# Kernel tuning notes

Hardware: AMD Instinct MI355X
Metric: run time of the kernel (lower is better)

The kernel has to match this reference:

```python
import jax, jax.numpy as jnp
import numpy as np

EPS = 1e-5
KEEP_FRAC = 0.925


def conv1x1(x, w, b):
    # x: [B,C,H,W], w: [O,C], b: [O]
    return jnp.einsum('bchw,oc->bohw', x, w) + b[None, :, None, None]


def adain_norm(x):
    m = x.mean(axis=(2, 3), keepdims=True)
    v = x.var(axis=(2, 3), keepdims=True)
    return (x - m) / jnp.sqrt(v + EPS)


def zca_norm(x):
    B, C, H, W = x.shape
    f = x.reshape(B, C, H * W)
    m = f.mean(axis=-1, keepdims=True)
    fc = f - m
    cov = jnp.einsum('bcn,bdn->bcd', fc, fc) / (H * W - 1) + EPS * jnp.eye(C, dtype=x.dtype)
    s, U = jnp.linalg.eigh(cov)
    Ud = U * (1.0 / jnp.sqrt(s + EPS))[:, None, :]          # U @ diag(s^-1/2)
    whiten = jnp.einsum('bce,bde->bcd', Ud, U)              # U diag U^T
    out = jnp.einsum('bcd,bdn->bcn', whiten, fc)
    return out.reshape(B, C, H, W)


def correlation_block(xq, yk, wf, bf, wg, bg):
    B, C, H, W = xq.shape
    f = conv1x1(xq, wf, bf).reshape(B, C, -1)   # [B,C,n_x]
    g = conv1x1(yk, wg, bg).reshape(B, C, -1)   # [B,C,n_y]
    energy = jnp.einsum('bcn,bcm->bnm', f, g)   # f^T g : [B,n_x,n_y]
    corr = jax.nn.softmax(energy, axis=-1)
    atten = corr.mean(axis=1, keepdims=True)    # mean over n_x -> [B,1,n_y]
    return corr, atten


def attn_mask(a):
    # a: [B,1,n]; zero the positions of the k smallest values (union over batch, as in torch)
    n = a.shape[2]
    k = int(n * KEEP_FRAC)
    idx = jnp.argsort(a, axis=2)[:, :, :k]                   # smallest k per (b, channel)
    mask = jnp.ones_like(a).at[:, :, idx.reshape(-1)].set(0.0)
    return mask


def corr_mask(mx, my):
    # mx: [B,1,n_x], my: [B,1,n_y] -> equality mask [B,n_x,n_y]
    return (mx[:, 0, :, None] == my[:, 0, None, :]).astype(mx.dtype)


def savanet_forward(x, y, f_w, f_b, g_w, g_b, sa_f_w, sa_f_b, sa_g_w, sa_g_b, h_w, h_b, out_w, out_b):
    B, C, H, W = x.shape
    n = H * W
    x_adain = adain_norm(x)
    y_adain = adain_norm(y)
    x_zca = zca_norm(x)
    y_zca = zca_norm(y)
    correlation, _ = correlation_block(x_adain, y_adain, f_w, f_b, g_w, g_b)
    _, atten_x = correlation_block(x_zca, x_zca, sa_f_w, sa_f_b, sa_g_w, sa_g_b)
    _, atten_y = correlation_block(y_zca, y_zca, sa_f_w, sa_f_b, sa_g_w, sa_g_b)
    mx = attn_mask(atten_x)
    my = attn_mask(atten_y)
    cmask = corr_mask(mx, my)                               # [B,n,n]
    correlation = cmask * correlation
    l1 = jnp.clip(jnp.abs(correlation).sum(axis=2, keepdims=True), 1e-12, None)
    correlation = correlation / l1                          # F.normalize(p=1, dim=2)
    h = conv1x1(y, h_w, h_b).reshape(B, C, n)               # [B,C,n_y]
    residual = jnp.einsum('bcm,bnm->bcn', h, correlation)   # h @ corr^T -> [B,C,n_x]
    residual = residual.reshape(B, C, H, W)
    residual = conv1x1(residual, out_w, out_b)
    output = x + residual
    return output, atten_x, atten_y


def setup_inputs() -> dict:
    key = jax.random.key(0)
    ks = jax.random.split(key, 10)
    B, C, H, W = 2, 512, 64, 64
    scale = 0.02
    d = {
        'x': jax.random.normal(ks[0], (B, C, H, W), dtype=jnp.float32),
        'y': jax.random.normal(ks[1], (B, C, H, W), dtype=jnp.float32),
        'f_w': jax.random.normal(ks[2], (C, C), dtype=jnp.float32) * scale,
        'f_b': jnp.zeros((C,), dtype=jnp.float32),
        'g_w': jax.random.normal(ks[3], (C, C), dtype=jnp.float32) * scale,
        'g_b': jnp.zeros((C,), dtype=jnp.float32),
        'sa_f_w': jax.random.normal(ks[4], (C, C), dtype=jnp.float32) * scale,
        'sa_f_b': jnp.zeros((C,), dtype=jnp.float32),
        'sa_g_w': jax.random.normal(ks[5], (C, C), dtype=jnp.float32) * scale,
        'sa_g_b': jnp.zeros((C,), dtype=jnp.float32),
        'h_w': jax.random.normal(ks[6], (C, C), dtype=jnp.float32) * scale,
        'h_b': jnp.zeros((C,), dtype=jnp.float32),
        'out_w': jax.random.normal(ks[7], (C, C), dtype=jnp.float32) * scale,
        'out_b': jnp.zeros((C,), dtype=jnp.float32),
    }
    return d


def reference(x, y, f_w, f_b, g_w, g_b, sa_f_w, sa_f_b, sa_g_w, sa_g_b, h_w, h_b, out_w, out_b):
    return savanet_forward(x, y, f_w, f_b, g_w, g_b, sa_f_w, sa_f_b, sa_g_w, sa_g_b, h_w, h_b, out_w, out_b)
```

## Files before the change

kernel.cpp:

```cpp
#include <hip/hip_runtime.h>
#include <cstdint>

static constexpr int B2 = 2;
static constexpr int C = 512;
static constexpr int N = 4096;
static constexpr long CN = (long)C * N;
static constexpr long NC = (long)N * C;
static constexpr long CC = (long)C * C;
static constexpr long NN = (long)N * N;
static constexpr float EPSC = 1e-5f;
static constexpr int KSEL = 308;
static constexpr int NS_ITERS = 4;

typedef __attribute__((ext_vector_type(8))) __bf16 bf16x8;
typedef __attribute__((ext_vector_type(4))) float f32x4;

__device__ __forceinline__ float wredSum(float v){
#pragma unroll
  for (int o = 32; o >= 1; o >>= 1) v += __shfl_xor(v, o, 64);
  return v;
}

__device__ __forceinline__ void gld16(const __bf16* g, __bf16* l){
  __builtin_amdgcn_global_load_lds(
      (const __attribute__((address_space(1))) void*)g,
      (__attribute__((address_space(3))) void*)l, 16, 0, 0);
}

__device__ __forceinline__ void splitw(float v, __bf16* ph, __bf16* pl, long o){
  __bf16 h = (__bf16)v;
  ph[o] = h;
  pl[o] = (__bf16)(v - (float)h);
}

template<int PASSES, int TMH, int OUTMODE, int ROWP>
__global__ __launch_bounds__(256) void k_mm(
    const __bf16* __restrict__ Ah, const __bf16* __restrict__ Al,
    const __bf16* __restrict__ Bh, const __bf16* __restrict__ Bl,
    float* __restrict__ Cf, __bf16* __restrict__ Coh, __bf16* __restrict__ Col,
    int Nn, int K, long sAz, long sBz, long sCz,
    float alpha, const float* __restrict__ alpha_ptr,
    const float* __restrict__ brow, long sBr,
    const float* __restrict__ bcol, long sBc,
    const float* __restrict__ c0p,
    const float* __restrict__ addsrc, long sAddz,
    float* __restrict__ Pm, float* __restrict__ Ps)
{
  constexpr int NB = (PASSES == 3) ? 4 : 2;
  constexpr int SB = (PASSES == 3) ? 2 : 1;
  __shared__ __align__(16) __bf16 sm[NB][128 * 32];
  __shared__ float pmx[2][128], psx[2][128];
  const int z = blockIdx.z;
  const int nwx = gridDim.x;
  int lin = blockIdx.y * nwx + blockIdx.x;
  const int nwg = nwx * gridDim.y;
  if ((nwg & 7) == 0){
    const int cpx = nwg >> 3;
    lin = (lin & 7) * cpx + (lin >> 3);
  }
  const int i0 = (lin % nwx) * 128;
  const int j0 = (lin / nwx) * 128;
  const int tid = threadIdx.x;
  const int lane = tid & 63;
  const int w = tid >> 6;
  const int wr = (w >> 1) * 64, wc = (w & 1) * 64;
  const int lr = lane & 15;
  const int g = lane >> 4;

  const __bf16* pAh = Ah + (long)z * sAz + (long)i0 * K;
  const __bf16* pBh = Bh + (long)z * sBz + (long)j0 * K;
  const __bf16* pAl = (PASSES == 3) ? (Al + (long)z * sAz + (long)i0 * K) : nullptr;
  const __bf16* pBl = (PASSES == 3) ? (Bl + (long)z * sBz + (long)j0 * K) : nullptr;

  f32x4 acc[4][4] = {};

  for (int kt = 0; kt < K; kt += 32){
#pragma unroll
    for (int p = 0; p < 2; ++p){
      const int t2 = p * 256 + tid;
      const int row = t2 >> 2;
      const int gs = (t2 & 3) ^ ((row >> 1) & 3);
      const long go = (long)row * K + kt + gs * 8;
      gld16(pAh + go, &sm[0][t2 * 8]);
      gld16(pBh + go, &sm[SB][t2 * 8]);
      if constexpr (PASSES == 3){
        gld16(pAl + go, &sm[1][t2 * 8]);
        gld16(pBl + go, &sm[3][t2 * 8]);
      }
    }
    __syncthreads();
    bf16x8 fa[4], fal[4], fb[4], fbl[4];
#pragma unroll
    for (int mi = 0; mi < 4; ++mi){
      const int row = wr + mi * 16 + lr;
      const int off = row * 32 + ((g ^ ((row >> 1) & 3)) * 8);
      fa[mi] = *(const bf16x8*)(&sm[0][off]);
      if constexpr (PASSES == 3) fal[mi] = *(const bf16x8*)(&sm[1][off]);
    }
#pragma unroll
    for (int ni = 0; ni < 4; ++ni){
      const int row = wc + ni * 16 + lr;
      const int off = row * 32 + ((g ^ ((row >> 1) & 3)) * 8);
      fb[ni] = *(const bf16x8*)(&sm[SB][off]);
      if constexpr (PASSES == 3) fbl[ni] = *(const bf16x8*)(&sm[3][off]);
    }
#pragma unroll
    for (int mi = 0; mi < 4; ++mi)
#pragma unroll
      for (int ni = 0; ni < 4; ++ni){
        acc[mi][ni] = __builtin_amdgcn_mfma_f32_16x16x32_bf16(fa[mi], fb[ni], acc[mi][ni], 0, 0, 0);
        if constexpr (PASSES == 3){
          acc[mi][ni] = __builtin_amdgcn_mfma_f32_16x16x32_bf16(fa[mi],  fbl[ni], acc[mi][ni], 0, 0, 0);
          acc[mi][ni] = __builtin_amdgcn_mfma_f32_16x16x32_bf16(fal[mi], fb[ni],  acc[mi][ni], 0, 0, 0);
        }
      }
    __syncthreads();
  }

  float al2 = alpha;
  if (alpha_ptr) al2 *= alpha_ptr[z];
  const float c0v = c0p ? c0p[z] : 0.f;
#pragma unroll
  for (int mi = 0; mi < 4; ++mi){
    float mrow[4] = {-3.4e38f, -3.4e38f, -3.4e38f, -3.4e38f};
    float srow[4] = {0.f, 0.f, 0.f, 0.f};
#pragma unroll
    for (int ni = 0; ni < 4; ++ni){
      const int col = j0 + wc + ni * 16 + lr;
      const float bc = (bcol ? bcol[z * sBc + col] : 0.f) + c0v;
#pragma unroll
      for (int j = 0; j < 4; ++j){
        const int row = i0 + wr + mi * 16 + g * 4 + j;
        float v = acc[mi][ni][j] * al2;
        if (TMH) v = (((row == col) ? 3.f : 0.f) - v) * 0.5f;
        if (brow) v += brow[z * sBr + row];
        v += bc;
        if (addsrc) v += addsrc[(long)z * sAddz + (long)row * Nn + col];
        const long o = (long)z * sCz + (long)row * Nn + col;
        if (OUTMODE == 0){ Cf[o] = v; }
        else if (OUTMODE == 1){ __bf16 h = (__bf16)v; Coh[o] = h; Col[o] = (__bf16)(v - (float)h); }
        else { Coh[o] = (__bf16)v; }
        if constexpr (ROWP){
          if (v > mrow[j]){ srow[j] *= __expf(mrow[j] - v); mrow[j] = v; }
          srow[j] += __expf(v - mrow[j]);
        }
      }
    }
    if constexpr (ROWP){
#pragma unroll
      for (int j = 0; j < 4; ++j){
        float m = mrow[j], s = srow[j];
#pragma unroll
        for (int o = 1; o <= 8; o <<= 1){
          const float mo = __shfl_xor(m, o, 64);
          const float so = __shfl_xor(s, o, 64);
          const float nm = fmaxf(m, mo);
          s = s * __expf(m - nm) + so * __expf(mo - nm);
          m = nm;
        }
        if (lr == 0){
          const int rl = wr + mi * 16 + g * 4 + j;
          pmx[w & 1][rl] = m;
          psx[w & 1][rl] = s;
        }
      }
    }
  }
  if constexpr (ROWP){
    __syncthreads();
    if (tid < 128){
      const float m0 = pmx[0][tid], s0 = psx[0][tid];
      const float m1 = pmx[1][tid], s1 = psx[1][tid];
      const float nm = fmaxf(m0, m1);
      const float s = s0 * __expf(m0 - nm) + s1 * __expf(m1 - nm);
      Pm[(long)(j0 >> 7) * N + i0 + tid] = nm;
      Ps[(long)(j0 >> 7) * N + i0 + tid] = s;
    }
  }
}

template<int TMH, int OUTMODE, int NSYZ>
__global__ __launch_bounds__(256) void k_mm64(
    const __bf16* __restrict__ Ah, const __bf16* __restrict__ Al,
    const __bf16* __restrict__ Bh, const __bf16* __restrict__ Bl,
    const __bf16* __restrict__ tH, const __bf16* __restrict__ tL,
    float* __restrict__ Cf, __bf16* __restrict__ Coh, __bf16* __restrict__ Col,
    int Nn, int K, long sAz, long sBz, long sCz, float alpha)
{
  __shared__ __align__(16) __bf16 sm[4][64 * 64];
  const int z = blockIdx.z;
  const __bf16 *bAh, *bAl, *bBh, *bBl;
  long oC;
  if constexpr (NSYZ){
    if (z < 4){
      bAh = Ah + (long)z * CC; bAl = Al + (long)z * CC;
      bBh = tH + (long)z * CC; bBl = tL + (long)z * CC;
      oC = (long)z * CC;
    } else {
      const int zz = z - 4;
      bAh = tH + (long)zz * CC; bAl = tL + (long)zz * CC;
      bBh = Ah + (long)(4 + zz) * CC; bBl = Al + (long)(4 + zz) * CC;
      oC = (long)(4 + zz) * CC;
    }
  } else {
    bAh = Ah + (long)z * sAz; bAl = Al + (long)z * sAz;
    bBh = Bh + (long)z * sBz; bBl = Bl + (long)z * sBz;
    oC = (long)z * sCz;
  }
  const int i0 = blockIdx.x * 64;
  const int j0 = blockIdx.y * 64;
  const int tid = threadIdx.x;
  const int lane = tid & 63;
  const int w = tid >> 6;
  const int wr = (w >> 1) * 32, wc = (w & 1) * 32;
  const int lr = lane & 15;
  const int g = lane >> 4;

  const __bf16* pAh = bAh + (long)i0 * K;
  const __bf16* pAl = bAl + (long)i0 * K;
  const __bf16* pBh = bBh + (long)j0 * K;
  const __bf16* pBl = bBl + (long)j0 * K;

  f32x4 acc[2][2] = {};

  for (int kt = 0; kt < K; kt += 64){
#pragma unroll
    for (int p = 0; p < 2; ++p){
      const int t2 = p * 256 + tid;
      const int row = t2 >> 3;
      const int gs = (t2 & 7) ^ (row & 7);
      const long go = (long)row * K + kt + gs * 8;
      gld16(pAh + go, &sm[0][t2 * 8]);
      gld16(pAl + go, &sm[1][t2 * 8]);
      gld16(pBh + go, &sm[2][t2 * 8]);
      gld16(pBl + go, &sm[3][t2 * 8]);
    }
    __syncthreads();
#pragma unroll
    for (int ks = 0; ks < 2; ++ks){
      bf16x8 fa[2], fal[2], fb[2], fbl[2];
#pragma unroll
      for (int mi = 0; mi < 2; ++mi){
        const int row = wr + mi * 16 + lr;
        const int off = row * 64 + (((ks * 4 + g) ^ (row & 7)) * 8);
        fa[mi]  = *(const bf16x8*)(&sm[0][off]);
        fal[mi] = *(const bf16x8*)(&sm[1][off]);
      }
#pragma unroll
      for (int ni = 0; ni < 2; ++ni){
        const int row = wc + ni * 16 + lr;
        const int off = row * 64 + (((ks * 4 + g) ^ (row & 7)) * 8);
        fb[ni]  = *(const bf16x8*)(&sm[2][off]);
        fbl[ni] = *(const bf16x8*)(&sm[3][off]);
      }
#pragma unroll
      for (int mi = 0; mi < 2; ++mi)
#pragma unroll
        for (int ni = 0; ni < 2; ++ni){
          acc[mi][ni] = __builtin_amdgcn_mfma_f32_16x16x32_bf16(fa[mi],  fb[ni],  acc[mi][ni], 0, 0, 0);
          acc[mi][ni] = __builtin_amdgcn_mfma_f32_16x16x32_bf16(fa[mi],  fbl[ni], acc[mi][ni], 0, 0, 0);
          acc[mi][ni] = __builtin_amdgcn_mfma_f32_16x16x32_bf16(fal[mi], fb[ni],  acc[mi][ni], 0, 0, 0);
        }
    }
    __syncthreads();
  }

#pragma unroll
  for (int mi = 0; mi < 2; ++mi){
#pragma unroll
    for (int ni = 0; ni < 2; ++ni){
      const int col = j0 + wc + ni * 16 + lr;
#pragma unroll
      for (int j = 0; j < 4; ++j){
        const int row = i0 + wr + mi * 16 + g * 4 + j;
        float v = acc[mi][ni][j] * alpha;
        if (TMH) v = (((row == col) ? 3.f : 0.f) - v) * 0.5f;
        const long o = oC + (long)row * Nn + col;
        if (OUTMODE == 0){ Cf[o] = v; }
        else { __bf16 h = (__bf16)v; Coh[o] = h; Col[o] = (__bf16)(v - (float)h); }
      }
    }
  }
}

__global__ __launch_bounds__(256) void k_pv(
    const __bf16* __restrict__ E, const __bf16* __restrict__ Bh,
    const float* __restrict__ rm, const float* __restrict__ rsc,
    const float* __restrict__ mxv, const float* __restrict__ myv,
    __bf16* __restrict__ resH)
{
  __shared__ __align__(16) __bf16 sa[64 * 64];
  __shared__ __align__(16) __bf16 sb[128 * 64];
  const int z = blockIdx.z;
  int lin = blockIdx.y * 64 + blockIdx.x;
  lin = (lin & 7) * 32 + (lin >> 3);
  const int n0 = (lin & 63) * 64;
  const int c0 = (lin >> 6) * 128;
  const int tid = threadIdx.x;
  const int lane = tid & 63;
  const int w = tid >> 6;
  const int wr = (w >> 1) * 32, wc = (w & 1) * 64;
  const int lr = lane & 15, g = lane >> 4;

  const __bf16* pe = E + (long)z * NN + (long)n0 * N;
  const __bf16* pB = Bh + (long)z * CN + (long)c0 * N;

  const int ar = tid >> 2;
  const int slot = tid & 3;
  const float rmv = rm[(long)z * N + n0 + ar];
  const float rsv = rsc[(long)z * N + n0 + ar];
  const float tgt = mxv[n0 + ar];
  const __bf16* per = pe + (long)ar * N;

  f32x4 acc[2][4] = {};

  for (int kt = 0; kt < N; kt += 64){
#pragma unroll
    for (int d = 0; d < 2; ++d){
      const int gd = slot * 2 + d;
      const bf16x8 ev = *(const bf16x8*)(per + kt + gd * 8);
      const float4 m0 = *(const float4*)(myv + kt + gd * 8);
      const float4 m1 = *(const float4*)(myv + kt + gd * 8 + 4);
      bf16x8 pk;
      pk[0] = (__bf16)((m0.x == tgt) ? __expf((float)ev[0] - rmv) * rsv : 0.f);
      pk[1] = (__bf16)((m0.y == tgt) ? __expf((float)ev[1] - rmv) * rsv : 0.f);
      pk[2] = (__bf16)((m0.z == tgt) ? __expf((float)ev[2] - rmv) * rsv : 0.f);
      pk[3] = (__bf16)((m0.w == tgt) ? __expf((float)ev[3] - rmv) * rsv : 0.f);
      pk[4] = (__bf16)((m1.x == tgt) ? __expf((float)ev[4] - rmv) * rsv : 0.f);
      pk[5] = (__bf16)((m1.y == tgt) ? __expf((float)ev[5] - rmv) * rsv : 0.f);
      pk[6] = (__bf16)((m1.z == tgt) ? __expf((float)ev[6] - rmv) * rsv : 0.f);
      pk[7] = (__bf16)((m1.w == tgt) ? __expf((float)ev[7] - rmv) * rsv : 0.f);
      *(bf16x8*)(&sa[ar * 64 + ((gd ^ (ar & 7)) * 8)]) = pk;
    }
#pragma unroll
    for (int p = 0; p < 4; ++p){
      const int t2 = p * 256 + tid;
      const int row = t2 >> 3;
      const int gs = (t2 & 7) ^ (row & 7);
      gld16(pB + (long)row * N + kt + gs * 8, &sb[t2 * 8]);
    }
    __syncthreads();
#pragma unroll
    for (int ks = 0; ks < 2; ++ks){
      bf16x8 fa[2], fb[4];
#pragma unroll
      for (int mi = 0; mi < 2; ++mi){
        const int row = wr + mi * 16 + lr;
        fa[mi] = *(const bf16x8*)(&sa[row * 64 + (((ks * 4 + g) ^ (row & 7)) * 8)]);
      }
#pragma unroll
      for (int ni = 0; ni < 4; ++ni){
        const int row = wc + ni * 16 + lr;
        fb[ni] = *(const bf16x8*)(&sb[row * 64 + (((ks * 4 + g) ^ (row & 7)) * 8)]);
      }
#pragma unroll
      for (int mi = 0; mi < 2; ++mi)
#pragma unroll
        for (int ni = 0; ni < 4; ++ni)
          acc[mi][ni] = __builtin_amdgcn_mfma_f32_16x16x32_bf16(fa[mi], fb[ni], acc[mi][ni], 0, 0, 0);
    }
    __syncthreads();
  }
#pragma unroll
  for (int mi = 0; mi < 2; ++mi)
#pragma unroll
    for (int ni = 0; ni < 4; ++ni){
      const int c = c0 + wc + ni * 16 + lr;
#pragma unroll
      for (int j = 0; j < 4; ++j){
        const int n = n0 + wr + mi * 16 + g * 4 + j;
        resH[(long)z * NC + (long)n * C + c] = (__bf16)acc[mi][ni][j];
      }
    }
}

__global__ __launch_bounds__(256) void k_wtw(const float* __restrict__ A, const float* __restrict__ B,
                                             float* __restrict__ C2, float alpha){
  __shared__ float sa[16][32], sb[16][32];
  const int i0 = blockIdx.x * 32, j0 = blockIdx.y * 32;
  const int t = threadIdx.x;
  const int ti = t & 15, tj = t >> 4;
  const int li = t & 31, lc = t >> 5;
  float acc[2][2] = {};
  for (int cb = 0; cb < C; cb += 16){
    sa[lc][li]     = A[(long)(cb + lc) * C + i0 + li];
    sa[lc + 8][li] = A[(long)(cb + lc + 8) * C + i0 + li];
    sb[lc][li]     = B[(long)(cb + lc) * C + j0 + li];
    sb[lc + 8][li] = B[(long)(cb + lc + 8) * C + j0 + li];
    __syncthreads();
#pragma unroll
    for (int c = 0; c < 16; ++c){
      const float a0 = sa[c][ti * 2], a1 = sa[c][ti * 2 + 1];
      const float b0 = sb[c][tj * 2], b1 = sb[c][tj * 2 + 1];
      acc[0][0] = fmaf(a0, b0, acc[0][0]); acc[0][1] = fmaf(a0, b1, acc[0][1]);
      acc[1][0] = fmaf(a1, b0, acc[1][0]); acc[1][1] = fmaf(a1, b1, acc[1][1]);
    }
    __syncthreads();
  }
#pragma unroll
  for (int r = 0; r < 2; ++r)
#pragma unroll
    for (int s = 0; s < 2; ++s)
      C2[(long)(i0 + ti * 2 + r) * C + j0 + tj * 2 + s] = acc[r][s] * alpha;
}

__global__ __launch_bounds__(256) void k_wtv(const float* __restrict__ W, const float* __restrict__ b,
                                             float* __restrict__ u){
  __shared__ float sb2[C];
  const int t = threadIdx.x;
  sb2[t] = b[t]; sb2[t + 256] = b[t + 256];
  __syncthreads();
  const int e = blockIdx.x * 256 + t;
  float acc = 0.f;
  for (int c = 0; c < C; ++c) acc = fmaf(W[(long)c * C + e], sb2[c], acc);
  u[e] = acc;
}

__global__ void k_dot2(const float* __restrict__ a1, const float* __restrict__ b1,
                       const float* __restrict__ a2, const float* __restrict__ b2,
                       float* __restrict__ c0m2, float* __restrict__ c0s4){
  const int t = threadIdx.x;
  float s1 = 0.f, s2 = 0.f;
  for (int i = t; i < C; i += 256){ s1 += a1[i] * b1[i]; s2 += a2[i] * b2[i]; }
  __shared__ float sh1[4], sh2[4];
  s1 = wredSum(s1); s2 = wredSum(s2);
  if ((t & 63) == 0){ sh1[t >> 6] = s1; sh2[t >> 6] = s2; }
  __syncthreads();
  if (t == 0){
    float d1 = sh1[0] + sh1[1] + sh1[2] + sh1[3];
    float d2 = sh2[0] + sh2[1] + sh2[2] + sh2[3];
    c0m2[0] = d1; c0m2[1] = d1;
    c0s4[0] = d2; c0s4[1] = d2; c0s4[2] = d2; c0s4[3] = d2;
  }
}

__global__ __launch_bounds__(256) void k_pixvec(const __bf16* __restrict__ X, const float* __restrict__ u,
                                                float* __restrict__ out){
  const int z = blockIdx.y;
  const int wv = threadIdx.x >> 6, lane = threadIdx.x & 63;
  const int n = blockIdx.x * 4 + wv;
  float acc = 0.f;
  for (int d = lane; d < C; d += 64) acc += (float)X[(long)z * NC + (long)n * C + d] * u[d];
  acc = wredSum(acc);
  if (lane == 0) out[(long)z * N + n] = acc;
}

__global__ __launch_bounds__(256) void k_stats(const float* __restrict__ x, const float* __restrict__ y,
                                               float* __restrict__ meanv, float* __restrict__ invs){
  const int bid = blockIdx.x;
  const int t = bid >> 9, c = bid & 511;
  const float* src = (t < 2 ? x : y) + (long)(t & 1) * CN + (long)c * N;
  const int tid = threadIdx.x;
  float s1 = 0.f, s2 = 0.f;
  for (int i = tid; i < N; i += 256){ float v = src[i]; s1 += v; s2 += v * v; }
  __shared__ float sh1[4], sh2[4];
  s1 = wredSum(s1); s2 = wredSum(s2);
  if ((tid & 63) == 0){ sh1[tid >> 6] = s1; sh2[tid >> 6] = s2; }
  __syncthreads();
  if (tid == 0){
    float m = (sh1[0] + sh1[1] + sh1[2] + sh1[3]) * (1.f / (float)N);
    float ex2 = (sh2[0] + sh2[1] + sh2[2] + sh2[3]) * (1.f / (float)N);
    float var = ex2 - m * m;
    meanv[t * C + c] = m;
    invs[t * C + c] = rsqrtf((var > 0.f ? var : 0.f) + EPSC);
  }
}

__global__ __launch_bounds__(256) void k_prep(const float* __restrict__ src,
                                              const float* __restrict__ meanv, const float* __restrict__ invs, int toff,
                                              __bf16* __restrict__ adH,
                                              __bf16* __restrict__ fcH, __bf16* __restrict__ fcL,
                                              __bf16* __restrict__ ccH, __bf16* __restrict__ ccL,
                                              __bf16* __restrict__ rwH){
  __shared__ float tile[64][65];
  const int z = blockIdx.z;
  const int n0 = blockIdx.x * 64;
  const int c0 = blockIdx.y * 64;
  const int tid = threadIdx.x;
  const int tx = tid & 63, ty = tid >> 6;
  const int tgt = toff + z;
#pragma unroll
  for (int it = 0; it < 16; ++it){
    const int cc = it * 4 + ty;
    const float v = src[(long)z * CN + (long)(c0 + cc) * N + n0 + tx];
    tile[cc][tx] = v;
    const float cen = v - meanv[tgt * C + c0 + cc];
    splitw(cen, ccH, ccL, (long)tgt * CN + (long)(c0 + cc) * N + n0 + tx);
  }
  __syncthreads();
  const float m = meanv[tgt * C + c0 + tx];
  const float r = invs[tgt * C + c0 + tx];
#pragma unroll
  for (int it = 0; it < 16; ++it){
    const int p = it * 4 + ty;
    const float v = tile[tx][p];
    const float cen = v - m;
    const long o = (long)z * NC + (long)(n0 + p) * C + c0 + tx;
    adH[o] = (__bf16)(cen * r);
    splitw(cen, fcH, fcL, (long)tgt * NC + (long)(n0 + p) * C + c0 + tx);
    if (rwH) rwH[o] = (__bf16)v;
  }
}

__global__ __launch_bounds__(256) void k_wcvt(const float* __restrict__ s, __bf16* __restrict__ h,
                                              __bf16* __restrict__ l, int n){
  int i = blockIdx.x * 256 + threadIdx.x;
  if (i < n) splitw(s[i], h, l, i);
}
__global__ __launch_bounds__(256) void k_wcvt_h(const float* __restrict__ s, __bf16* __restrict__ h, int n){
  int i = blockIdx.x * 256 + threadIdx.x;
  if (i < n) h[i] = (__bf16)s[i];
}

__global__ void k_diag(float* __restrict__ cov){
  const int z = blockIdx.x, t = threadIdx.x;
  for (int i = t; i < C; i += 256) cov[(long)z * CC + (long)i * C + i] += 2.f * EPSC;
}

__global__ __launch_bounds__(256) void k_powit(const float* __restrict__ cov,
                                               float* __restrict__ invt, float* __restrict__ invsqt){
  __shared__ float v[C], red[4];
  const int z = blockIdx.x, t = threadIdx.x;
  const float* A = cov + (long)z * CC;
  const int j0 = t, j1 = t + 256;
  v[j0] = 1.f + 0.0003f * (float)j0;
  v[j1] = 1.f + 0.0003f * (float)j1;
  __syncthreads();
  float lam = 1.f;
  for (int it = 0; it < 4; ++it){
    float w0a = 0.f, w0b = 0.f, w1a = 0.f, w1b = 0.f;
#pragma unroll 8
    for (int c = 0; c < C; c += 2){
      const float vc0 = v[c], vc1 = v[c + 1];
      w0a = fmaf(A[(long)c * C + j0], vc0, w0a);
      w1a = fmaf(A[(long)c * C + j1], vc0, w1a);
      w0b = fmaf(A[(long)(c + 1) * C + j0], vc1, w0b);
      w1b = fmaf(A[(long)(c + 1) * C + j1], vc1, w1b);
    }
    const float w0 = w0a + w0b, w1 = w1a + w1b;
    float s = w0 * w0 + w1 * w1;
    s = wredSum(s);
    if ((t & 63) == 0) red[t >> 6] = s;
    __syncthreads();
    const float nrm = sqrtf(red[0] + red[1] + red[2] + red[3]);
    lam = nrm;
    const float inv = 1.f / nrm;
    v[j0] = w0 * inv;
    v[j1] = w1 * inv;
    __syncthreads();
  }
  if (t == 0){
    const float tt = 1.02f * lam;
    invt[z] = 1.f / tt;
    invsqt[z] = rsqrtf(tt);
  }
}

__global__ __launch_bounds__(256) void k_ns_init(const float* __restrict__ cov, const float* __restrict__ invt,
                                                 __bf16* __restrict__ h, __bf16* __restrict__ l,
                                                 __bf16* __restrict__ cph, __bf16* __restrict__ cpl){
  const int r = blockIdx.x, z = blockIdx.y;
  const long base = (long)z * CC + (long)r * C;
  const float it = invt[z];
  for (int i = threadIdx.x; i < C; i += 256){
    const float v = cov[base + i] * it;
    splitw(v, h, l, base + i);
    splitw(v, cph, cpl, base + i);
    h[4 * CC + base + i] = (__bf16)((i == r) ? 1.f : 0.f);
    l[4 * CC + base + i] = (__bf16)0.f;
  }
}

__global__ __launch_bounds__(256) void k_prowmerge(const float* __restrict__ Pm, const float* __restrict__ Ps,
                                                   float* __restrict__ rm, float* __restrict__ rsc){
  const int row = blockIdx.x * 256 + threadIdx.x;
  float m = -3.4e38f, s = 0.f;
#pragma unroll 4
  for (int p = 0; p < 32; ++p){
    const float mp = Pm[(long)p * N + row];
    const float sp = Ps[(long)p * N + row];
    const float nm = fmaxf(m, mp);
    s = s * __expf(m - nm) + sp * __expf(mp - nm);
    m = nm;
  }
  rm[row] = m;
  rsc[row] = 1.f / s;
}

__global__ __launch_bounds__(256) void k_colaccum(const float* __restrict__ E, const float* __restrict__ rowmax,
                                                  const float* __restrict__ rowscale, float* __restrict__ partials){
  const int j = (blockIdx.x * 256 + threadIdx.x) * 4;
  const int r0 = blockIdx.y * 128;
  float4 acc = {0.f, 0.f, 0.f, 0.f};
  for (int r2 = r0; r2 < r0 + 128; ++r2){
    const float4 e = *reinterpret_cast<const float4*>(E + (long)r2 * N + j);
    const float rmv = rowmax[r2], rsv = rowscale[r2];
    acc.x += __expf(e.x - rmv) * rsv;
    acc.y += __expf(e.y - rmv) * rsv;
    acc.z += __expf(e.z - rmv) * rsv;
    acc.w += __expf(e.w - rmv) * rsv;
  }
  *reinterpret_cast<float4*>(partials + (long)blockIdx.y * N + j) = acc;
}

__global__ __launch_bounds__(256) void k_colreduce(const float* __restrict__ partials, float* __restrict__ att){
  const int j = blockIdx.x * 256 + threadIdx.x;
  float s = 0.f;
#pragma unroll 4
  for (int p = 0; p < 32; ++p) s += partials[(long)p * N + j];
  att[j] = s * (1.f / (float)N);
}

__global__ __launch_bounds__(256) void k_rowstats1(
    const __bf16* __restrict__ E, const float* __restrict__ mx, const float* __restrict__ my,
    float* __restrict__ rowmax, float* __restrict__ rowscale)
{
  const int zz = blockIdx.y;
  const int r0 = blockIdx.x * 16;
  const int tid = threadIdx.x;
  const int rr = tid >> 4;
  const int l16 = tid & 15;
  const int row = r0 + rr;
  const __bf16* pe = E + (long)zz * NN + (long)row * N;
  const float target = mx[row];
  float m = -3.4e38f, s = 0.f, sm = 0.f;
  for (int i = l16 * 8; i < N; i += 128){
    const bf16x8 ev = *(const bf16x8*)(pe + i);
    const float4 w0 = *(const float4*)(my + i);
    const float4 w1 = *(const float4*)(my + i + 4);
    float e[8];
#pragma unroll
    for (int k = 0; k < 8; ++k) e[k] = (float)ev[k];
    float mv = fmaxf(fmaxf(fmaxf(e[0], e[1]), fmaxf(e[2], e[3])),
                     fmaxf(fmaxf(e[4], e[5]), fmaxf(e[6], e[7])));
    if (mv > m){ const float sc = __expf(m - mv); s *= sc; sm *= sc; m = mv; }
    float x0 = __expf(e[0] - m), x1 = __expf(e[1] - m), x2 = __expf(e[2] - m), x3 = __expf(e[3] - m);
    float x4 = __expf(e[4] - m), x5 = __expf(e[5] - m), x6 = __expf(e[6] - m), x7 = __expf(e[7] - m);
    s += ((x0 + x1) + (x2 + x3)) + ((x4 + x5) + (x6 + x7));
    if (w0.x == target) sm += x0;
    if (w0.y == target) sm += x1;
    if (w0.z == target) sm += x2;
    if (w0.w == target) sm += x3;
    if (w1.x == target) sm += x4;
    if (w1.y == target) sm += x5;
    if (w1.z == target) sm += x6;
    if (w1.w == target) sm += x7;
  }
#pragma unroll
  for (int o = 8; o >= 1; o >>= 1){
    const float mo = __shfl_xor(m, o, 64);
    const float so = __shfl_xor(s, o, 64);
    const float smo = __shfl_xor(sm, o, 64);
    const float nm = fmaxf(m, mo);
    const float sc0 = __expf(m - nm), sc1 = __expf(mo - nm);
    s = s * sc0 + so * sc1;
    sm = sm * sc0 + smo * sc1;
    m = nm;
  }
  if (l16 == 0){
    float l1 = sm / s;
    if (l1 < 1e-12f) l1 = 1e-12f;
    rowscale[(long)zz * N + row] = 1.f / (s * l1);
    rowmax[(long)zz * N + row] = m;
  }
}

__global__ __launch_bounds__(256) void k_radix(const float* __restrict__ a, float* __restrict__ thr){
  __shared__ unsigned int vals[N];
  __shared__ float shc[4];
  __shared__ unsigned int p_sh;
  __shared__ int k_sh;
  const float* pa = a + (long)blockIdx.x * N;
  const int tid = threadIdx.x;
  for (int i = tid; i < N; i += 256) vals[i] = __float_as_uint(pa[i]);
  if (tid == 0){ p_sh = 0u; k_sh = KSEL; }
  __syncthreads();
  for (int b = 31; b >= 0; --b){
    const unsigned int bit = 1u << b;
    const unsigned int above = (b == 31) ? 0u : ~((bit << 1) - 1u);
    const unsigned int p = p_sh;
    int cnt = 0;
    for (int i = tid; i < N; i += 256){
      unsigned int v = vals[i];
      if ((v & above) == p && (v & bit)) cnt++;
    }
    float cf = wredSum((float)cnt);
    if ((tid & 63) == 0) shc[tid >> 6] = cf;
    __syncthreads();
    if (tid == 0){
      int c1 = (int)(shc[0] + shc[1] + shc[2] + shc[3] + 0.5f);
      if (k_sh <= c1) p_sh = p | bit;
      else k_sh -= c1;
    }
    __syncthreads();
  }
  if (tid == 0) thr[blockIdx.x] = __uint_as_float(p_sh);
}

__global__ __launch_bounds__(256) void k_mask(const float* __restrict__ ax, const float* __restrict__ ay,
                                              const float* __restrict__ thr, float* __restrict__ mx,
                                              float* __restrict__ my){
  int j = blockIdx.x * 256 + threadIdx.x;
  mx[j] = (ax[j] >= thr[0] && ax[N + j] >= thr[1]) ? 1.f : 0.f;
  my[j] = (ay[j] >= thr[2] && ay[N + j] >= thr[3]) ? 1.f : 0.f;
}

extern "C" void kernel_launch(void* const* d_in, const int* in_sizes, int n_in,
                              void* d_out, int out_size, void* d_ws, size_t ws_size,
                              hipStream_t stream)
{
  const float* x     = (const float*)d_in[0];
  const float* y     = (const float*)d_in[1];
  const float* f_w   = (const float*)d_in[2];
  const float* f_b   = (const float*)d_in[3];
  const float* g_w   = (const float*)d_in[4];
  const float* g_b   = (const float*)d_in[5];
  const float* saf_w = (const float*)d_in[6];
  const float* saf_b = (const float*)d_in[7];
  const float* sag_w = (const float*)d_in[8];
  const float* sag_b = (const float*)d_in[9];
  const float* h_w   = (const float*)d_in[10];
  const float* h_b   = (const float*)d_in[11];
  const float* ow    = (const float*)d_in[12];
  const float* ob    = (const float*)d_in[13];

  const size_t MBy = 1ull << 20;
  char* base = (char*)d_ws;
  if (ws_size < 206 * MBy) return;
  auto F  = [&](size_t off){ return (float*)(base + off); };
  auto Bp = [&](size_t off){ return (__bf16*)(base + off); };

  float *E0 = F(0);
  __bf16 *Ebf = Bp(0);
  __bf16 *ccH = Bp(0), *ccL = Bp(16*MBy);
  float  *covb = F(32*MBy);
  __bf16 *zpolH = Bp(36*MBy), *zpolL = Bp(38*MBy);
  __bf16 *covPH = Bp(40*MBy), *covPL = Bp(42*MBy);
  float  *KsTf = F(44*MBy), *K2tf = F(45*MBy);
  __bf16 *KsTH = Bp(46*MBy), *KsTL = Bp(46*MBy + 512*1024);
  __bf16 *K2tH = Bp(47*MBy), *hwH = Bp(47*MBy + 512*1024);
  __bf16 *tpH = Bp(48*MBy), *tpL = Bp(50*MBy);
  __bf16 *xaH = Bp(64*MBy);
  __bf16 *xzH = Bp(64*MBy), *xzL = Bp(80*MBy);
  __bf16 *ypmH = Bp(96*MBy);
  __bf16 *AsH = Bp(96*MBy), *AsL = Bp(112*MBy);
  __bf16 *fcH = Bp(128*MBy), *fcL = Bp(144*MBy);
  __bf16 *resH = Bp(128*MBy);
  __bf16 *nsAh = Bp(160*MBy), *nsAl = Bp(164*MBy);
  __bf16 *nsBh = Bp(168*MBy), *nsBl = Bp(172*MBy);
  __bf16 *A2H = Bp(176*MBy);
  __bf16 *yaH = Bp(184*MBy);
  __bf16 *hH  = Bp(192*MBy);
  __bf16 *owH = Bp(200*MBy);
  size_t so = 200 * MBy + 512 * 1024;
  auto SF = [&](size_t bytes){ float* p = F(so); so += bytes; return p; };
  float *meanv = SF(8*1024), *invs = SF(8*1024);
  float *rm = SF(32*1024), *rsc = SF(32*1024);
  float *mxv = SF(16*1024), *myv = SF(16*1024);
  float *rvec2 = SF(32*1024), *cvec2 = SF(32*1024);
  float *rvS = SF(64*1024), *cvS = SF(64*1024);
  float *u1m = SF(2*1024), *u2m = SF(2*1024), *u1s = SF(2*1024), *u2s = SF(2*1024);
  float *c0m2 = SF(64), *c0s4 = SF(64), *thr = SF(64);
  float *invt = SF(64), *invsqt = SF(64);
  float *partials = F(201*MBy);
  float *Pm = F(201*MBy + 512*1024);
  float *Ps = F(201*MBy + 1024*1024);

  float* outm = (float*)d_out;
  float* attx = outm + B2 * CN;
  float* atty = attx + (long)B2 * N;

  k_stats<<<dim3(4 * C), dim3(256), 0, stream>>>(x, y, meanv, invs);
  k_prep<<<dim3(64, 8, 2), dim3(256), 0, stream>>>(x, meanv, invs, 0, xaH, fcH, fcL, ccH, ccL, nullptr);
  k_prep<<<dim3(64, 8, 2), dim3(256), 0, stream>>>(y, meanv, invs, 2, yaH, fcH, fcL, ccH, ccL, ypmH);

  k_wtw<<<dim3(16, 16), dim3(256), 0, stream>>>(sag_w, saf_w, KsTf, 1.f);
  k_wtw<<<dim3(16, 16), dim3(256), 0, stream>>>(g_w, f_w, K2tf, 1.f);
  {
    const int nb = (int)(CC / 256);
    k_wcvt<<<nb, 256, 0, stream>>>(KsTf, KsTH, KsTL, (int)CC);
    k_wcvt_h<<<nb, 256, 0, stream>>>(K2tf, K2tH, (int)CC);
    k_wcvt_h<<<nb, 256, 0, stream>>>(h_w, hwH, (int)CC);
    k_wcvt_h<<<nb, 256, 0, stream>>>(ow, owH, (int)CC);
  }
  k_wtv<<<dim3(2), dim3(256), 0, stream>>>(g_w, f_b, u1m);
  k_wtv<<<dim3(2), dim3(256), 0, stream>>>(f_w, g_b, u2m);
  k_wtv<<<dim3(2), dim3(256), 0, stream>>>(sag_w, saf_b, u1s);
  k_wtv<<<dim3(2), dim3(256), 0, stream>>>(saf_w, sag_b, u2s);
  k_dot2<<<dim3(1), dim3(256), 0, stream>>>(f_b, g_b, saf_b, sag_b, c0m2, c0s4);
  k_pixvec<<<dim3(N / 4, 2), dim3(256), 0, stream>>>(xaH, u2m, rvec2);
  k_pixvec<<<dim3(N / 4, 2), dim3(256), 0, stream>>>(yaH, u1m, cvec2);

  k_mm64<0,0,0><<<dim3(8, 8, 4), dim3(256), 0, stream>>>(
      ccH, ccL, ccH, ccL, nullptr, nullptr, covb, nullptr, nullptr, C, N, CN, CN, CC, 1.f / (float)(N - 1));
  k_diag<<<dim3(4), dim3(256), 0, stream>>>(covb);
  k_powit<<<dim3(4), dim3(256), 0, stream>>>(covb, invt, invsqt);

  k_mm<1,0,2,0><<<dim3(32, 4, 2), dim3(256), 0, stream>>>(xaH, nullptr, K2tH, nullptr, nullptr, A2H, nullptr,
      C, C, NC, 0, NC, 1.f, nullptr, nullptr, 0, nullptr, 0, nullptr, nullptr, 0, nullptr, nullptr);
  k_mm<1,0,2,0><<<dim3(4, 32, 2), dim3(256), 0, stream>>>(hwH, nullptr, ypmH, nullptr, nullptr, hH, nullptr,
      N, C, 0, NC, CN, 1.f, nullptr, h_b, 0, nullptr, 0, nullptr, nullptr, 0, nullptr, nullptr);

  k_ns_init<<<dim3(C, 4), dim3(256), 0, stream>>>(covb, invt, nsAh, nsAl, covPH, covPL);
  __bf16 *cah = nsAh, *cal = nsAl, *cbh = nsBh, *cbl = nsBl;
  for (int it = 0; it < NS_ITERS; ++it){
    k_mm64<1,1,0><<<dim3(8, 8, 4), dim3(256), 0, stream>>>(
        cah + 4*CC, cal + 4*CC, cah, cal, nullptr, nullptr, nullptr, tpH, tpL, C, C, CC, CC, CC, 1.f);
    k_mm64<0,1,1><<<dim3(8, 8, 8), dim3(256), 0, stream>>>(
        cah, cal, nullptr, nullptr, tpH, tpL, nullptr, cbh, cbl, C, C, CC, CC, CC, 1.f);
    __bf16* t;
    t = cah; cah = cbh; cbh = t;
    t = cal; cal = cbl; cbl = t;
  }
  k_mm64<0,1,0><<<dim3(8, 8, 4), dim3(256), 0, stream>>>(
      cah + 4*CC, cal + 4*CC, cah + 4*CC, cal + 4*CC, nullptr, nullptr, nullptr, tpH, tpL, C, C, CC, CC, CC, 1.f);
  k_mm64<1,1,0><<<dim3(8, 8, 4), dim3(256), 0, stream>>>(
      covPH, covPL, tpH, tpL, nullptr, nullptr, nullptr, cbh, cbl, C, C, CC, CC, CC, 1.f);
  k_mm64<0,1,0><<<dim3(8, 8, 4), dim3(256), 0, stream>>>(
      cah + 4*CC, cal + 4*CC, cbh, cbl, nullptr, nullptr, nullptr, zpolH, zpolL, C, C, CC, CC, CC, 1.f);

  k_mm<3,0,1,0><<<dim3(32, 4, 4), dim3(256), 0, stream>>>(fcH, fcL, zpolH, zpolL, nullptr, xzH, xzL,
      C, C, NC, CC, NC, 1.f, invsqt, nullptr, 0, nullptr, 0, nullptr, nullptr, 0, nullptr, nullptr);

  k_pixvec<<<dim3(N / 4, 4), dim3(256), 0, stream>>>(xzH, u2s, rvS);
  k_pixvec<<<dim3(N / 4, 4), dim3(256), 0, stream>>>(xzH, u1s, cvS);
  k_mm<3,0,1,0><<<dim3(32, 4, 4), dim3(256), 0, stream>>>(xzH, xzL, KsTH, KsTL, nullptr, AsH, AsL,
      C, C, NC, 0, NC, 1.f, nullptr, nullptr, 0, nullptr, 0, nullptr, nullptr, 0, nullptr, nullptr);

  for (int z = 0; z < 4; ++z){
    k_mm<3,0,0,1><<<dim3(32, 32, 1), dim3(256), 0, stream>>>(AsH + (long)z*NC, AsL + (long)z*NC,
        xzH + (long)z*NC, xzL + (long)z*NC, E0, nullptr, nullptr,
        N, C, 0, 0, 0, 1.f, nullptr, rvS + (long)z*N, 0, cvS + (long)z*N, 0, c0s4, nullptr, 0, Pm, Ps);
    k_prowmerge<<<dim3(16), dim3(256), 0, stream>>>(Pm, Ps, rm, rsc);
    k_colaccum<<<dim3(4, 32), dim3(256), 0, stream>>>(E0, rm, rsc, partials);
    k_colreduce<<<dim3(16), dim3(256), 0, stream>>>(partials, (z < 2 ? attx : atty) + (long)(z & 1) * N);
  }

  k_radix<<<dim3(2), dim3(256), 0, stream>>>(attx, thr);
  k_radix<<<dim3(2), dim3(256), 0, stream>>>(atty, thr + 2);
  k_mask<<<dim3(16), dim3(256), 0, stream>>>(attx, atty, thr, mxv, myv);

  k_mm<1,0,2,0><<<dim3(32, 32, 2), dim3(256), 0, stream>>>(A2H, nullptr, yaH, nullptr, nullptr, Ebf, nullptr,
      N, C, NC, NC, NN, 1.f, nullptr, rvec2, N, cvec2, N, c0m2, nullptr, 0, nullptr, nullptr);
  k_rowstats1<<<dim3(N / 16, 2), dim3(256), 0, stream>>>(Ebf, mxv, myv, rm, rsc);
  k_pv<<<dim3(64, 4, 2), dim3(256), 0, stream>>>(Ebf, hH, rm, rsc, mxv, myv, resH);
  k_mm<1,0,0,0><<<dim3(4, 32, 2), dim3(256), 0, stream>>>(owH, nullptr, resH, nullptr, outm, nullptr, nullptr,
      N, C, 0, NC, CN, 1.f, nullptr, ob, 0, nullptr, 0, nullptr, x, CN, nullptr, nullptr);
}
```

Measured before the change: 1.272 ms.

## Fuse masked softmax row statistics into energy GEMM epilogue and widen column accumulation

The mutual-attention energy GEMM epilogue now computes per-tile online-softmax max, sum and mask-matched sum. It writes these as partials that a small merge kernel combines into row max and scale, replacing the separate kernel that re-read the whole bf16 energy matrix. The row statistics are computed from the bf16-rounded values so they stay consistent with the stored matrix. The column-accumulation kernel also splits rows into 128 groups instead of 32 for more parallelism, which gives a longer final reduction. The cost is extra epilogue work and registers in the GEMM.

```diff
diff --git a/kernel.cpp b/kernel.cpp
--- a/kernel.cpp
+++ b/kernel.cpp
@@ -44,12 +44,13 @@
     const float* __restrict__ bcol, long sBc,
     const float* __restrict__ c0p,
     const float* __restrict__ addsrc, long sAddz,
-    float* __restrict__ Pm, float* __restrict__ Ps)
+    float* __restrict__ Pm, float* __restrict__ Ps, float* __restrict__ Pq,
+    const float* __restrict__ mxp, const float* __restrict__ myp)
 {
   constexpr int NB = (PASSES == 3) ? 4 : 2;
   constexpr int SB = (PASSES == 3) ? 2 : 1;
   __shared__ __align__(16) __bf16 sm[NB][128 * 32];
-  __shared__ float pmx[2][128], psx[2][128];
+  __shared__ float pmx[2][128], psx[2][128], pqx[2][128];
   const int z = blockIdx.z;
   const int nwx = gridDim.x;
   int lin = blockIdx.y * nwx + blockIdx.x;
@@ -124,10 +125,12 @@
   for (int mi = 0; mi < 4; ++mi){
     float mrow[4] = {-3.4e38f, -3.4e38f, -3.4e38f, -3.4e38f};
     float srow[4] = {0.f, 0.f, 0.f, 0.f};
+    float qrow[4] = {0.f, 0.f, 0.f, 0.f};
 #pragma unroll
     for (int ni = 0; ni < 4; ++ni){
       const int col = j0 + wc + ni * 16 + lr;
       const float bc = (bcol ? bcol[z * sBc + col] : 0.f) + c0v;
+      const float mycol = (ROWP == 2) ? myp[col] : 0.f;
 #pragma unroll
       for (int j = 0; j < 4; ++j){
         const int row = i0 + wr + mi * 16 + g * 4 + j;
@@ -139,42 +142,61 @@
         const long o = (long)z * sCz + (long)row * Nn + col;
         if (OUTMODE == 0){ Cf[o] = v; }
         else if (OUTMODE == 1){ __bf16 h = (__bf16)v; Coh[o] = h; Col[o] = (__bf16)(v - (float)h); }
-        else { Coh[o] = (__bf16)v; }
-        if constexpr (ROWP){
-          if (v > mrow[j]){ srow[j] *= __expf(mrow[j] - v); mrow[j] = v; }
-          srow[j] += __expf(v - mrow[j]);
+        else { __bf16 h = (__bf16)v; Coh[o] = h; if (ROWP == 2) v = (float)h; }
+        if constexpr (ROWP >= 1){
+          if (v > mrow[j]){
+            const float sc = __expf(mrow[j] - v);
+            srow[j] *= sc;
+            if constexpr (ROWP == 2) qrow[j] *= sc;
+            mrow[j] = v;
+          }
+          const float ev = __expf(v - mrow[j]);
+          srow[j] += ev;
+          if constexpr (ROWP == 2){
+            if (mycol == mxp[row]) qrow[j] += ev;
+          }
         }
       }
     }
-    if constexpr (ROWP){
+    if constexpr (ROWP >= 1){
 #pragma unroll
       for (int j = 0; j < 4; ++j){
-        float m = mrow[j], s = srow[j];
+        float m = mrow[j], s = srow[j], q = qrow[j];
 #pragma unroll
         for (int o = 1; o <= 8; o <<= 1){
           const float mo = __shfl_xor(m, o, 64);
           const float so = __shfl_xor(s, o, 64);
+          float qo = 0.f;
+          if constexpr (ROWP == 2) qo = __shfl_xor(q, o, 64);
           const float nm = fmaxf(m, mo);
-          s = s * __expf(m - nm) + so * __expf(mo - nm);
+          const float c0_ = __expf(m - nm), c1_ = __expf(mo - nm);
+          s = s * c0_ + so * c1_;
+          if constexpr (ROWP == 2) q = q * c0_ + qo * c1_;
           m = nm;
         }
         if (lr == 0){
           const int rl = wr + mi * 16 + g * 4 + j;
           pmx[w & 1][rl] = m;
           psx[w & 1][rl] = s;
+          if constexpr (ROWP == 2) pqx[w & 1][rl] = q;
         }
       }
     }
   }
-  if constexpr (ROWP){
+  if constexpr (ROWP >= 1){
     __syncthreads();
     if (tid < 128){
       const float m0 = pmx[0][tid], s0 = psx[0][tid];
       const float m1 = pmx[1][tid], s1 = psx[1][tid];
       const float nm = fmaxf(m0, m1);
-      const float s = s0 * __expf(m0 - nm) + s1 * __expf(m1 - nm);
-      Pm[(long)(j0 >> 7) * N + i0 + tid] = nm;
-      Ps[(long)(j0 >> 7) * N + i0 + tid] = s;
+      const float c0_ = __expf(m0 - nm), c1_ = __expf(m1 - nm);
+      const float s = s0 * c0_ + s1 * c1_;
+      const long po = (long)(z * 32 + (j0 >> 7)) * N + i0 + tid;
+      Pm[po] = nm;
+      Ps[po] = s;
+      if constexpr (ROWP == 2){
+        Pq[po] = pqx[0][tid] * c0_ + pqx[1][tid] * c1_;
+      }
     }
   }
 }
@@ -587,12 +609,35 @@
   rsc[row] = 1.f / s;
 }
 
+__global__ __launch_bounds__(256) void k_prowmerge_m(const float* __restrict__ Pm, const float* __restrict__ Ps,
+                                                     const float* __restrict__ Pq,
+                                                     float* __restrict__ rm, float* __restrict__ rsc){
+  const int z = blockIdx.y;
+  const int row = blockIdx.x * 256 + threadIdx.x;
+  float m = -3.4e38f, s = 0.f, q = 0.f;
+#pragma unroll 4
+  for (int p = 0; p < 32; ++p){
+    const long idx = (long)(z * 32 + p) * N + row;
+    const float mp = Pm[idx], sp = Ps[idx], qp = Pq[idx];
+    const float nm = fmaxf(m, mp);
+    const float c0_ = __expf(m - nm), c1_ = __expf(mp - nm);
+    s = s * c0_ + sp * c1_;
+    q = q * c0_ + qp * c1_;
+    m = nm;
+  }
+  float l1 = q / s;
+  if (l1 < 1e-12f) l1 = 1e-12f;
+  rsc[(long)z * N + row] = 1.f / (s * l1);
+  rm[(long)z * N + row] = m;
+}
+
 __global__ __launch_bounds__(256) void k_colaccum(const float* __restrict__ E, const float* __restrict__ rowmax,
                                                   const float* __restrict__ rowscale, float* __restrict__ partials){
   const int j = (blockIdx.x * 256 + threadIdx.x) * 4;
-  const int r0 = blockIdx.y * 128;
+  const int r0 = blockIdx.y * 32;
   float4 acc = {0.f, 0.f, 0.f, 0.f};
-  for (int r2 = r0; r2 < r0 + 128; ++r2){
+#pragma unroll 4
+  for (int r2 = r0; r2 < r0 + 32; ++r2){
     const float4 e = *reinterpret_cast<const float4*>(E + (long)r2 * N + j);
     const float rmv = rowmax[r2], rsv = rowscale[r2];
     acc.x += __expf(e.x - rmv) * rsv;
@@ -606,63 +651,9 @@
 __global__ __launch_bounds__(256) void k_colreduce(const float* __restrict__ partials, float* __restrict__ att){
   const int j = blockIdx.x * 256 + threadIdx.x;
   float s = 0.f;
-#pragma unroll 4
-  for (int p = 0; p < 32; ++p) s += partials[(long)p * N + j];
+#pragma unroll 8
+  for (int p = 0; p < 128; ++p) s += partials[(long)p * N + j];
   att[j] = s * (1.f / (float)N);
-}
-
-__global__ __launch_bounds__(256) void k_rowstats1(
-    const __bf16* __restrict__ E, const float* __restrict__ mx, const float* __restrict__ my,
-    float* __restrict__ rowmax, float* __restrict__ rowscale)
-{
-  const int zz = blockIdx.y;
-  const int r0 = blockIdx.x * 16;
-  const int tid = threadIdx.x;
-  const int rr = tid >> 4;
-  const int l16 = tid & 15;
-  const int row = r0 + rr;
-  const __bf16* pe = E + (long)zz * NN + (long)row * N;
-  const float target = mx[row];
-  float m = -3.4e38f, s = 0.f, sm = 0.f;
-  for (int i = l16 * 8; i < N; i += 128){
-    const bf16x8 ev = *(const bf16x8*)(pe + i);
-    const float4 w0 = *(const float4*)(my + i);
-    const float4 w1 = *(const float4*)(my + i + 4);
-    float e[8];
-#pragma unroll
-    for (int k = 0; k < 8; ++k) e[k] = (float)ev[k];
-    float mv = fmaxf(fmaxf(fmaxf(e[0], e[1]), fmaxf(e[2], e[3])),
-                     fmaxf(fmaxf(e[4], e[5]), fmaxf(e[6], e[7])));
-    if (mv > m){ const float sc = __expf(m - mv); s *= sc; sm *= sc; m = mv; }
-    float x0 = __expf(e[0] - m), x1 = __expf(e[1] - m), x2 = __expf(e[2] - m), x3 = __expf(e[3] - m);
-    float x4 = __expf(e[4] - m), x5 = __expf(e[5] - m), x6 = __expf(e[6] - m), x7 = __expf(e[7] - m);
-    s += ((x0 + x1) + (x2 + x3)) + ((x4 + x5) + (x6 + x7));
-    if (w0.x == target) sm += x0;
-    if (w0.y == target) sm += x1;
-    if (w0.z == target) sm += x2;
-    if (w0.w == target) sm += x3;
-    if (w1.x == target) sm += x4;
-    if (w1.y == target) sm += x5;
-    if (w1.z == target) sm += x6;
-    if (w1.w == target) sm += x7;
-  }
-#pragma unroll
-  for (int o = 8; o >= 1; o >>= 1){
-    const float mo = __shfl_xor(m, o, 64);
-    const float so = __shfl_xor(s, o, 64);
-    const float smo = __shfl_xor(sm, o, 64);
-    const float nm = fmaxf(m, mo);
-    const float sc0 = __expf(m - nm), sc1 = __expf(mo - nm);
-    s = s * sc0 + so * sc1;
-    sm = sm * sc0 + smo * sc1;
-    m = nm;
-  }
-  if (l16 == 0){
-    float l1 = sm / s;
-    if (l1 < 1e-12f) l1 = 1e-12f;
-    rowscale[(long)zz * N + row] = 1.f / (s * l1);
-    rowmax[(long)zz * N + row] = m;
-  }
 }
 
 __global__ __launch_bounds__(256) void k_radix(const float* __restrict__ a, float* __restrict__ thr){
@@ -725,6 +716,7 @@
   const float* ob    = (const float*)d_in[13];
 
   const size_t MBy = 1ull << 20;
+  const size_t KBy = 1ull << 10;
   char* base = (char*)d_ws;
   if (ws_size < 206 * MBy) return;
   auto F  = [&](size_t off){ return (float*)(base + off); };
@@ -737,8 +729,8 @@
   __bf16 *zpolH = Bp(36*MBy), *zpolL = Bp(38*MBy);
   __bf16 *covPH = Bp(40*MBy), *covPL = Bp(42*MBy);
   float  *KsTf = F(44*MBy), *K2tf = F(45*MBy);
-  __bf16 *KsTH = Bp(46*MBy), *KsTL = Bp(46*MBy + 512*1024);
-  __bf16 *K2tH = Bp(47*MBy), *hwH = Bp(47*MBy + 512*1024);
+  __bf16 *KsTH = Bp(46*MBy), *KsTL = Bp(46*MBy + 512*KBy);
+  __bf16 *K2tH = Bp(47*MBy), *hwH = Bp(47*MBy + 512*KBy);
   __bf16 *tpH = Bp(48*MBy), *tpL = Bp(50*MBy);
   __bf16 *xaH = Bp(64*MBy);
   __bf16 *xzH = Bp(64*MBy), *xzL = Bp(80*MBy);
@@ -752,19 +744,20 @@
   __bf16 *yaH = Bp(184*MBy);
   __bf16 *hH  = Bp(192*MBy);
   __bf16 *owH = Bp(200*MBy);
-  size_t so = 200 * MBy + 512 * 1024;
+  size_t so = 200 * MBy + 512 * KBy;
   auto SF = [&](size_t bytes){ float* p = F(so); so += bytes; return p; };
-  float *meanv = SF(8*1024), *invs = SF(8*1024);
-  float *rm = SF(32*1024), *rsc = SF(32*1024);
-  float *mxv = SF(16*1024), *myv = SF(16*1024);
-  float *rvec2 = SF(32*1024), *cvec2 = SF(32*1024);
-  float *rvS = SF(64*1024), *cvS = SF(64*1024);
-  float *u1m = SF(2*1024), *u2m = SF(2*1024), *u1s = SF(2*1024), *u2s = SF(2*1024);
+  float *meanv = SF(8*KBy), *invs = SF(8*KBy);
+  float *rm = SF(32*KBy), *rsc = SF(32*KBy);
+  float *mxv = SF(16*KBy), *myv = SF(16*KBy);
+  float *rvec2 = SF(32*KBy), *cvec2 = SF(32*KBy);
+  float *rvS = SF(64*KBy), *cvS = SF(64*KBy);
+  float *u1m = SF(2*KBy), *u2m = SF(2*KBy), *u1s = SF(2*KBy), *u2s = SF(2*KBy);
   float *c0m2 = SF(64), *c0s4 = SF(64), *thr = SF(64);
   float *invt = SF(64), *invsqt = SF(64);
   float *partials = F(201*MBy);
-  float *Pm = F(201*MBy + 512*1024);
-  float *Ps = F(201*MBy + 1024*1024);
+  float *Pm = F(203*MBy);
+  float *Ps = F(204*MBy);
+  float *Pq = F(205*MBy);
 
   float* outm = (float*)d_out;
   float* attx = outm + B2 * CN;
@@ -797,9 +790,11 @@
   k_powit<<<dim3(4), dim3(256), 0, stream>>>(covb, invt, invsqt);
 
   k_mm<1,0,2,0><<<dim3(32, 4, 2), dim3(256), 0, stream>>>(xaH, nullptr, K2tH, nullptr, nullptr, A2H, nullptr,
-      C, C, NC, 0, NC, 1.f, nullptr, nullptr, 0, nullptr, 0, nullptr, nullptr, 0, nullptr, nullptr);
+      C, C, NC, 0, NC, 1.f, nullptr, nullptr, 0, nullptr, 0, nullptr, nullptr, 0,
+      nullptr, nullptr, nullptr, nullptr, nullptr);
   k_mm<1,0,2,0><<<dim3(4, 32, 2), dim3(256), 0, stream>>>(hwH, nullptr, ypmH, nullptr, nullptr, hH, nullptr,
-      N, C, 0, NC, CN, 1.f, nullptr, h_b, 0, nullptr, 0, nullptr, nullptr, 0, nullptr, nullptr);
+      N, C, 0, NC, CN, 1.f, nullptr, h_b, 0, nullptr, 0, nullptr, nullptr, 0,
+      nullptr, nullptr, nullptr, nullptr, nullptr);
 
   k_ns_init<<<dim3(C, 4), dim3(256), 0, stream>>>(covb, invt, nsAh, nsAl, covPH, covPL);
   __bf16 *cah = nsAh, *cal = nsAl, *cbh = nsBh, *cbl = nsBl;
@@ -820,19 +815,22 @@
       cah + 4*CC, cal + 4*CC, cbh, cbl, nullptr, nullptr, nullptr, zpolH, zpolL, C, C, CC, CC, CC, 1.f);
 
   k_mm<3,0,1,0><<<dim3(32, 4, 4), dim3(256), 0, stream>>>(fcH, fcL, zpolH, zpolL, nullptr, xzH, xzL,
-      C, C, NC, CC, NC, 1.f, invsqt, nullptr, 0, nullptr, 0, nullptr, nullptr, 0, nullptr, nullptr);
+      C, C, NC, CC, NC, 1.f, invsqt, nullptr, 0, nullptr, 0, nullptr, nullptr, 0,
+      nullptr, nullptr, nullptr, nullptr, nullptr);
 
   k_pixvec<<<dim3(N / 4, 4), dim3(256), 0, stream>>>(xzH, u2s, rvS);
   k_pixvec<<<dim3(N / 4, 4), dim3(256), 0, stream>>>(xzH, u1s, cvS);
   k_mm<3,0,1,0><<<dim3(32, 4, 4), dim3(256), 0, stream>>>(xzH, xzL, KsTH, KsTL, nullptr, AsH, AsL,
-      C, C, NC, 0, NC, 1.f, nullptr, nullptr, 0, nullptr, 0, nullptr, nullptr, 0, nullptr, nullptr);
+      C, C, NC, 0, NC, 1.f, nullptr, nullptr, 0, nullptr, 0, nullptr, nullptr, 0,
+      nullptr, nullptr, nullptr, nullptr, nullptr);
 
   for (int z = 0; z < 4; ++z){
     k_mm<3,0,0,1><<<dim3(32, 32, 1), dim3(256), 0, stream>>>(AsH + (long)z*NC, AsL + (long)z*NC,
         xzH + (long)z*NC, xzL + (long)z*NC, E0, nullptr, nullptr,
-        N, C, 0, 0, 0, 1.f, nullptr, rvS + (long)z*N, 0, cvS + (long)z*N, 0, c0s4, nullptr, 0, Pm, Ps);
+        N, C, 0, 0, 0, 1.f, nullptr, rvS + (long)z*N, 0, cvS + (long)z*N, 0, c0s4, nullptr, 0,
+        Pm, Ps, nullptr, nullptr, nullptr);
     k_prowmerge<<<dim3(16), dim3(256), 0, stream>>>(Pm, Ps, rm, rsc);
-    k_colaccum<<<dim3(4, 32), dim3(256), 0, stream>>>(E0, rm, rsc, partials);
+    k_colaccum<<<dim3(4, 128), dim3(256), 0, stream>>>(E0, rm, rsc, partials);
     k_colreduce<<<dim3(16), dim3(256), 0, stream>>>(partials, (z < 2 ? attx : atty) + (long)(z & 1) * N);
   }
 
@@ -840,10 +838,12 @@
   k_radix<<<dim3(2), dim3(256), 0, stream>>>(atty, thr + 2);
   k_mask<<<dim3(16), dim3(256), 0, stream>>>(attx, atty, thr, mxv, myv);
 
-  k_mm<1,0,2,0><<<dim3(32, 32, 2), dim3(256), 0, stream>>>(A2H, nullptr, yaH, nullptr, nullptr, Ebf, nullptr,
-      N, C, NC, NC, NN, 1.f, nullptr, rvec2, N, cvec2, N, c0m2, nullptr, 0, nullptr, nullptr);
-  k_rowstats1<<<dim3(N / 16, 2), dim3(256), 0, stream>>>(Ebf, mxv, myv, rm, rsc);
+  k_mm<1,0,2,2><<<dim3(32, 32, 2), dim3(256), 0, stream>>>(A2H, nullptr, yaH, nullptr, nullptr, Ebf, nullptr,
+      N, C, NC, NC, NN, 1.f, nullptr, rvec2, N, cvec2, N, c0m2, nullptr, 0,
+      Pm, Ps, Pq, mxv, myv);
+  k_prowmerge_m<<<dim3(16, 2), dim3(256), 0, stream>>>(Pm, Ps, Pq, rm, rsc);
   k_pv<<<dim3(64, 4, 2), dim3(256), 0, stream>>>(Ebf, hH, rm, rsc, mxv, myv, resH);
   k_mm<1,0,0,0><<<dim3(4, 32, 2), dim3(256), 0, stream>>>(owH, nullptr, resH, nullptr, outm, nullptr, nullptr,
-      N, C, 0, NC, CN, 1.f, nullptr, ob, 0, nullptr, 0, nullptr, x, CN, nullptr, nullptr);
-}
+      N, C, 0, NC, CN, 1.f, nullptr, ob, 0, nullptr, 0, nullptr, x, CN,
+      nullptr, nullptr, nullptr, nullptr, nullptr);
+}
```

Result: no change. 1.293 ms (+1.7%).
